# Kernel optimization log

Measured on AMD Instinct MI355X. Metric: run time of the kernel, lower is better.

Reference implementation:

```python
import jax, jax.numpy as jnp
import numpy as np

B, C, H, W = 8, 64, 64, 64


def setup_inputs() -> dict:
    key = jax.random.key(0)
    ks = jax.random.split(key, 8)
    s = 1.0 / np.sqrt(C)  # keep logits in a reasonable range
    return {
        "x": jax.random.normal(ks[0], (B, C, H, W), dtype=jnp.float32),
        "Wf": jax.random.normal(ks[1], (C, C), dtype=jnp.float32) * s,
        "bf": jax.random.normal(ks[2], (C,), dtype=jnp.float32) * s,
        "Wg": jax.random.normal(ks[3], (C, C), dtype=jnp.float32) * s,
        "bg": jax.random.normal(ks[4], (C,), dtype=jnp.float32) * s,
        "Wh": jax.random.normal(ks[5], (C, C), dtype=jnp.float32) * s,
        "bh": jax.random.normal(ks[6], (C,), dtype=jnp.float32) * s,
        "gamma": jax.random.normal(ks[7], (1,), dtype=jnp.float32),
    }


def reference(x, Wf, bf, Wg, bg, Wh, bh, gamma):
    b, c, h, w = x.shape
    n = h * w
    xf = x.reshape(b, c, n)  # [B, C, N]
    # 1x1 convs == per-pixel channel GEMMs
    f = jnp.einsum("oc,bcn->bon", Wf, xf) + bf[None, :, None]  # [B, C, N]
    g = jnp.einsum("oc,bcn->bon", Wg, xf) + bg[None, :, None]
    hh = jnp.einsum("oc,bcn->bon", Wh, xf) + bh[None, :, None]
    # att_in[b, i, j] = f[b, :, i] . g[b, :, j]  (f_x permuted then bmm with g_x)
    att = jax.nn.softmax(jnp.einsum("bci,bcj->bij", f, g), axis=-1)  # [B, N, N]
    # torch.bmm(h_x, attention): out[b, c, j] = sum_i h[b, c, i] * att[b, i, j]
    out = jnp.einsum("bci,bij->bcj", hh, att).reshape(b, c, h, w)
    return gamma[0] * out + x
```

## Files before the change

### kernel.cpp

```cpp
#include <hip/hip_runtime.h>

#define BB 8
#define CC 64
#define NN 4096
#define NIC 4
#define JCH 8
#define LOG2E 1.4426950408889634f

typedef float f32x4  __attribute__((ext_vector_type(4)));
typedef float f32x16 __attribute__((ext_vector_type(16)));
typedef _Float16 half8_t __attribute__((ext_vector_type(8)));
typedef int int4v __attribute__((ext_vector_type(4)));


__global__ __launch_bounds__(256, 4) void qkv_kernel(
    const float* __restrict__ x,
    const float* __restrict__ Wf, const float* __restrict__ bf,
    const float* __restrict__ Wg, const float* __restrict__ bg,
    const float* __restrict__ Wh, const float* __restrict__ bh,
    _Float16* __restrict__ fT, _Float16* __restrict__ gT,
    _Float16* __restrict__ hT)
{
    __shared__ float xbuf[64][136];

    const int tid  = threadIdx.x;
    const int lane = tid & 63;
    const int wv   = tid >> 6;
    const int l31  = lane & 31;
    const int q5   = lane >> 5;
    const int n0   = blockIdx.x * 128;
    const int b    = blockIdx.y;
    const int z    = blockIdx.z;
    const float* W    = (z == 0) ? Wf : ((z == 1) ? Wg : Wh);
    const float* bias = (z == 0) ? bf : ((z == 1) ? bg : bh);

    {
        const int row = tid >> 2;
        const float* src = x + (size_t)(b * CC + row) * NN + n0 + (tid & 3) * 4;
#pragma unroll
        for (int k = 0; k < 8; ++k) {
            const f32x4 v = *(const f32x4*)(src + k * 16);
            *(f32x4*)&xbuf[row][(tid & 3) * 4 + k * 16] = v;
        }
    }
    __syncthreads();

    const int px = wv * 32 + l31;
    half8_t xf[4];
#pragma unroll
    for (int kc = 0; kc < 4; ++kc) {
        const int kb = kc * 16 + q5 * 8;
        int4v p;
#pragma unroll
        for (int h2 = 0; h2 < 4; ++h2) {
            p[h2] = __builtin_bit_cast(int, __builtin_amdgcn_cvt_pkrtz(
                xbuf[kb + h2 * 2][px], xbuf[kb + h2 * 2 + 1][px]));
        }
        xf[kc] = __builtin_bit_cast(half8_t, p);
    }

    half8_t wf[2][4];
#pragma unroll
    for (int ot = 0; ot < 2; ++ot) {
        const float* wrow = W + (size_t)(ot * 32 + l31) * CC;
#pragma unroll
        for (int kc = 0; kc < 4; ++kc) {
            const f32x4 w0 = *(const f32x4*)(wrow + kc * 16 + q5 * 8);
            const f32x4 w1 = *(const f32x4*)(wrow + kc * 16 + q5 * 8 + 4);
            int4v p;
            p[0] = __builtin_bit_cast(int, __builtin_amdgcn_cvt_pkrtz(w0[0], w0[1]));
            p[1] = __builtin_bit_cast(int, __builtin_amdgcn_cvt_pkrtz(w0[2], w0[3]));
            p[2] = __builtin_bit_cast(int, __builtin_amdgcn_cvt_pkrtz(w1[0], w1[1]));
            p[3] = __builtin_bit_cast(int, __builtin_amdgcn_cvt_pkrtz(w1[2], w1[3]));
            wf[ot][kc] = __builtin_bit_cast(half8_t, p);
        }
    }

    if (z < 2) {
        const float scale = (z == 0) ? LOG2E : 1.0f;
        _Float16* dstT = (z == 0) ? fT : gT;
#pragma unroll
        for (int ot = 0; ot < 2; ++ot) {
            f32x16 acc = {};
#pragma unroll
            for (int kc = 0; kc < 4; ++kc)
                acc = __builtin_amdgcn_mfma_f32_32x32x16_f16(xf[kc], wf[ot][kc], acc, 0, 0, 0);
            const float bv = bias[ot * 32 + l31];
#pragma unroll
            for (int r = 0; r < 16; ++r) {
                const int prow = (r & 3) + 8 * (r >> 2) + 4 * q5;
                const int n = n0 + wv * 32 + prow;
                dstT[(size_t)(b * NN + n) * CC + ot * 32 + l31] =
                    (_Float16)((acc[r] + bv) * scale);
            }
        }
    } else {
        _Float16* hbase = hT + ((size_t)(b * (NN / 32) + (n0 + wv * 32) / 32) * CC) * 32;
#pragma unroll
        for (int ot = 0; ot < 2; ++ot) {
            f32x16 acc = {};
#pragma unroll
            for (int kc = 0; kc < 4; ++kc)
                acc = __builtin_amdgcn_mfma_f32_32x32x16_f16(wf[ot][kc], xf[kc], acc, 0, 0, 0);
#pragma unroll
            for (int rb = 0; rb < 4; ++rb) {
                const f32x4 b4 = *(const f32x4*)(bias + ot * 32 + rb * 8 + q5 * 4);
#pragma unroll
                for (int k = 0; k < 4; ++k) {
                    const int c = ot * 32 + rb * 8 + q5 * 4 + k;
                    hbase[(size_t)c * 32 + l31] = (_Float16)(acc[rb * 4 + k] + b4[k]);
                }
            }
        }
    }
}

__global__ __launch_bounds__(256, 4) void stats_kernel(
    const _Float16* __restrict__ fT, const _Float16* __restrict__ gT,
    float* __restrict__ lpart)
{
    __shared__ _Float16 gbuf[2][64][72];

    const int lane = threadIdx.x & 63;
    const int wv   = threadIdx.x >> 6;
    const int b    = blockIdx.y;
    const int jc   = blockIdx.z;
    const int i0   = blockIdx.x * 128 + wv * 32;
    const int l31  = lane & 31;
    const int q5   = lane >> 5;

    half8_t a[4];
    const _Float16* fa = fT + (size_t)(b * NN + i0 + l31) * CC + q5 * 8;
#pragma unroll
    for (int kc = 0; kc < 4; ++kc) a[kc] = *(const half8_t*)(fa + kc * 16);

    const _Float16* gchunk = gT + (size_t)(b * NN + jc * (NN / JCH)) * CC;
    const int T = NN / JCH / 64;

    const int srow = wv * 16 + (lane >> 3);
    const int scol = (lane & 7) * 8;

    {
        const half8_t v0 = *(const half8_t*)(gchunk + (size_t)srow * CC + scol);
        const half8_t v1 = *(const half8_t*)(gchunk + (size_t)(srow + 8) * CC + scol);
        *(half8_t*)&gbuf[0][srow][scol] = v0;
        *(half8_t*)&gbuf[0][srow + 8][scol] = v1;
    }
    __syncthreads();

    float l16[16];
#pragma unroll
    for (int r = 0; r < 16; ++r) l16[r] = 0.f;

    for (int t = 0; t < T; ++t) {
        const int buf = t & 1;
        const bool pf = (t + 1 < T);
        half8_t p0, p1;
        if (pf) {
            const _Float16* src = gchunk + (size_t)((t + 1) * 64 + srow) * CC + scol;
            p0 = *(const half8_t*)(src);
            p1 = *(const half8_t*)(src + 8 * CC);
        }
#pragma unroll
        for (int js = 0; js < 2; ++js) {
            const _Float16* grow = &gbuf[buf][js * 32 + l31][0] + q5 * 8;
            f32x16 s = {};
#pragma unroll
            for (int kc = 0; kc < 4; ++kc) {
                const half8_t bfr = *(const half8_t*)(grow + kc * 16);
                s = __builtin_amdgcn_mfma_f32_32x32x16_f16(a[kc], bfr, s, 0, 0, 0);
            }
#pragma unroll
            for (int r = 0; r < 16; ++r) l16[r] += __builtin_exp2f(s[r]);
        }
        if (pf) {
            *(half8_t*)&gbuf[buf ^ 1][srow][scol] = p0;
            *(half8_t*)&gbuf[buf ^ 1][srow + 8][scol] = p1;
        }
        __syncthreads();
    }

#pragma unroll
    for (int r = 0; r < 16; ++r) {
#pragma unroll
        for (int off = 1; off < 32; off <<= 1)
            l16[r] += __shfl_xor(l16[r], off);
    }

    if (l31 == 0) {
        float* lp = lpart + (size_t)jc * BB * NN + b * NN + i0;
#pragma unroll
        for (int rb = 0; rb < 4; ++rb) {
            f32x4 v;
#pragma unroll
            for (int k = 0; k < 4; ++k) v[k] = l16[rb * 4 + k];
            *(f32x4*)(lp + rb * 8 + q5 * 4) = v;
        }
    }
}

__global__ __launch_bounds__(256) void rmerge_kernel(
    const float* __restrict__ lpart, float* __restrict__ nbias)
{
    const int idx = blockIdx.x * 256 + threadIdx.x;
    float s = 0.f;
#pragma unroll
    for (int jc = 0; jc < JCH; ++jc) s += lpart[(size_t)jc * BB * NN + idx];
    nbias[idx] = -__builtin_log2f(s);
}

__global__ __launch_bounds__(256, 2) void attn_kernel(
    const _Float16* __restrict__ fT, const _Float16* __restrict__ gT,
    const _Float16* __restrict__ hT, const float* __restrict__ nbias,
    _Float16* __restrict__ pout)
{
    __shared__ _Float16 fbuf[2][64][72];
    __shared__ _Float16 hbuf[2][64][72];

    const int lane = threadIdx.x & 63;
    const int wv   = threadIdx.x >> 6;
    const int b    = blockIdx.y;
    const int ic   = blockIdx.z;
    const int l31  = lane & 31;
    const int q5   = lane >> 5;
    const int jbase = blockIdx.x * 256 + wv * 64;

    half8_t bg[2][4];
#pragma unroll
    for (int jt = 0; jt < 2; ++jt) {
        const _Float16* grow = gT + (size_t)(b * NN + jbase + jt * 32 + l31) * CC + q5 * 8;
#pragma unroll
        for (int kc = 0; kc < 4; ++kc) bg[jt][kc] = *(const half8_t*)(grow + kc * 16);
    }

    f32x16 acc[2][2] = {};

    const int ichunk = NN / NIC;
    const int ibase  = ic * ichunk;
    const _Float16* fchunk = fT + ((size_t)b * NN + ibase) * CC;
    const _Float16* hchunk = hT + ((size_t)(b * (NN / 32) + ibase / 32) * CC) * 32;
    const float*    nb     = nbias + b * NN + ibase;
    const int T = ichunk / 64;

    const int tid    = threadIdx.x;
    const int frow_s = tid >> 2;
    const int fcol_s = (tid & 3) * 16;
    const int hrow_s = tid >> 2;
    const int hcol_s = (tid & 3) * 8;

    {
        const half8_t f0 = *(const half8_t*)(fchunk + (size_t)frow_s * CC + fcol_s);
        const half8_t f1 = *(const half8_t*)(fchunk + (size_t)frow_s * CC + fcol_s + 8);
        const half8_t h0 = *(const half8_t*)(hchunk + tid * 8);
        const half8_t h1 = *(const half8_t*)(hchunk + 2048 + tid * 8);
        *(half8_t*)&fbuf[0][frow_s][fcol_s]     = f0;
        *(half8_t*)&fbuf[0][frow_s][fcol_s + 8] = f1;
        *(half8_t*)&hbuf[0][hrow_s][hcol_s]      = h0;
        *(half8_t*)&hbuf[0][hrow_s][32 + hcol_s] = h1;
    }
    __syncthreads();

    for (int t = 0; t < T; ++t) {
        const int buf = t & 1;
        const bool pf = (t + 1 < T);
        half8_t pf0, pf1, ph0, ph1;
        if (pf) {
            const _Float16* fsrc = fchunk + (size_t)((t + 1) * 64 + frow_s) * CC + fcol_s;
            const _Float16* hsrc = hchunk + (size_t)(t + 1) * 4096 + tid * 8;
            pf0 = *(const half8_t*)(fsrc);
            pf1 = *(const half8_t*)(fsrc + 8);
            ph0 = *(const half8_t*)(hsrc);
            ph1 = *(const half8_t*)(hsrc + 2048);
        }

#pragma unroll
        for (int ih = 0; ih < 2; ++ih) {
            f32x16 s0;
#pragma unroll
            for (int rb = 0; rb < 4; ++rb) {
                const f32x4 n4 = *(const f32x4*)(nb + t * 64 + ih * 32 + rb * 8 + q5 * 4);
#pragma unroll
                for (int k = 0; k < 4; ++k) s0[rb * 4 + k] = n4[k];
            }
            f32x16 s1 = s0;
            const _Float16* frow = &fbuf[buf][ih * 32 + l31][0] + q5 * 8;
#pragma unroll
            for (int kc = 0; kc < 4; ++kc) {
                const half8_t af = *(const half8_t*)(frow + kc * 16);
                s0 = __builtin_amdgcn_mfma_f32_32x32x16_f16(af, bg[0][kc], s0, 0, 0, 0);
                s1 = __builtin_amdgcn_mfma_f32_32x32x16_f16(af, bg[1][kc], s1, 0, 0, 0);
            }

            half8_t B[2][2];
#pragma unroll
            for (int jt = 0; jt < 2; ++jt) {
                const f32x16& s = jt ? s1 : s0;
                int e[8];
#pragma unroll
                for (int r8 = 0; r8 < 8; ++r8) {
                    e[r8] = __builtin_bit_cast(int, __builtin_amdgcn_cvt_pkrtz(
                        __builtin_exp2f(s[r8 * 2]), __builtin_exp2f(s[r8 * 2 + 1])));
                }
                const int sA = q5 ? e[0] : e[2];
                const int sB = q5 ? e[1] : e[3];
                const int sC = q5 ? e[4] : e[6];
                const int sD = q5 ? e[5] : e[7];
                const int rA = __shfl_xor(sA, 32, 64);
                const int rB = __shfl_xor(sB, 32, 64);
                const int rC = __shfl_xor(sC, 32, 64);
                const int rD = __shfl_xor(sD, 32, 64);
                int4v b0, b1;
                b0[0] = q5 ? rA   : e[0];
                b0[1] = q5 ? rB   : e[1];
                b0[2] = q5 ? e[2] : rA;
                b0[3] = q5 ? e[3] : rB;
                b1[0] = q5 ? rC   : e[4];
                b1[1] = q5 ? rD   : e[5];
                b1[2] = q5 ? e[6] : rC;
                b1[3] = q5 ? e[7] : rD;
                B[jt][0] = __builtin_bit_cast(half8_t, b0);
                B[jt][1] = __builtin_bit_cast(half8_t, b1);
            }

#pragma unroll
            for (int ct = 0; ct < 2; ++ct) {
                const half8_t ah0 = *(const half8_t*)(&hbuf[buf][ct * 32 + l31][0] + ih * 32 + q5 * 8);
                const half8_t ah1 = *(const half8_t*)(&hbuf[buf][ct * 32 + l31][0] + ih * 32 + 16 + q5 * 8);
                acc[0][ct] = __builtin_amdgcn_mfma_f32_32x32x16_f16(ah0, B[0][0], acc[0][ct], 0, 0, 0);
                acc[0][ct] = __builtin_amdgcn_mfma_f32_32x32x16_f16(ah1, B[0][1], acc[0][ct], 0, 0, 0);
                acc[1][ct] = __builtin_amdgcn_mfma_f32_32x32x16_f16(ah0, B[1][0], acc[1][ct], 0, 0, 0);
                acc[1][ct] = __builtin_amdgcn_mfma_f32_32x32x16_f16(ah1, B[1][1], acc[1][ct], 0, 0, 0);
            }
        }

        if (pf) {
            *(half8_t*)&fbuf[buf ^ 1][frow_s][fcol_s]     = pf0;
            *(half8_t*)&fbuf[buf ^ 1][frow_s][fcol_s + 8] = pf1;
            *(half8_t*)&hbuf[buf ^ 1][hrow_s][hcol_s]      = ph0;
            *(half8_t*)&hbuf[buf ^ 1][hrow_s][32 + hcol_s] = ph1;
        }
        __syncthreads();
    }

    _Float16* pb_out = pout + (((size_t)ic * BB + b) * CC) * NN;
#pragma unroll
    for (int jt = 0; jt < 2; ++jt) {
        const int j = jbase + jt * 32 + l31;
#pragma unroll
        for (int ct = 0; ct < 2; ++ct) {
#pragma unroll
            for (int r = 0; r < 16; ++r) {
                const int c = ct * 32 + (r & 3) + 8 * (r >> 2) + 4 * q5;
                pb_out[(size_t)c * NN + j] = (_Float16)acc[jt][ct][r];
            }
        }
    }
}

__global__ __launch_bounds__(256) void combine_kernel(
    const float* __restrict__ x, const float* __restrict__ gammap,
    const _Float16* __restrict__ pout, float* __restrict__ out)
{
    const float gam = gammap[0];
    const size_t i8 = ((size_t)blockIdx.x * 256 + threadIdx.x) * 8;
    const size_t TOT = (size_t)BB * CC * NN;

    float s[8] = {0.f, 0.f, 0.f, 0.f, 0.f, 0.f, 0.f, 0.f};
#pragma unroll
    for (int ic = 0; ic < NIC; ++ic) {
        const half8_t p = *(const half8_t*)(pout + ic * TOT + i8);
#pragma unroll
        for (int k = 0; k < 8; ++k) s[k] += (float)p[k];
    }
    const f32x4 x0 = *(const f32x4*)(x + i8);
    const f32x4 x1 = *(const f32x4*)(x + i8 + 4);
    f32x4 o0, o1;
#pragma unroll
    for (int k = 0; k < 4; ++k) { o0[k] = gam * s[k] + x0[k]; o1[k] = gam * s[k + 4] + x1[k]; }
    *(f32x4*)(out + i8) = o0;
    *(f32x4*)(out + i8 + 4) = o1;
}

extern "C" void kernel_launch(void* const* d_in, const int* in_sizes, int n_in,
                              void* d_out, int out_size, void* d_ws, size_t ws_size,
                              hipStream_t stream) {
    const float* x     = (const float*)d_in[0];
    const float* Wf    = (const float*)d_in[1];
    const float* bf    = (const float*)d_in[2];
    const float* Wg    = (const float*)d_in[3];
    const float* bg    = (const float*)d_in[4];
    const float* Wh    = (const float*)d_in[5];
    const float* bh    = (const float*)d_in[6];
    const float* gamma = (const float*)d_in[7];
    float* out = (float*)d_out;

    const size_t TOT = (size_t)BB * CC * NN;
    _Float16* fT   = (_Float16*)d_ws;
    _Float16* gT   = fT + TOT;
    _Float16* hT   = gT + TOT;
    _Float16* pout = hT + TOT;
    float* lpart   = (float*)(pout + (size_t)NIC * TOT);
    float* nbias   = lpart + (size_t)JCH * BB * NN;

    qkv_kernel<<<dim3(NN / 128, BB, 3), 256, 0, stream>>>(
        x, Wf, bf, Wg, bg, Wh, bh, fT, gT, hT);
    stats_kernel<<<dim3(NN / 128, BB, JCH), 256, 0, stream>>>(fT, gT, lpart);
    rmerge_kernel<<<dim3(BB * NN / 256), 256, 0, stream>>>(lpart, nbias);
    attn_kernel<<<dim3(NN / 256, BB, NIC), 256, 0, stream>>>(fT, gT, hT, nbias, pout);
    combine_kernel<<<dim3(TOT / (256 * 8)), 256, 0, stream>>>(x, gamma, pout, out);
}
```

Baseline: 177.7 us.

## Fuse Q/K/V projections into one block so x is loaded once

New measurement: 177.5 us. Within noise of the previous version (-0.1%).

```diff
diff --git a/kernel.cpp b/kernel.cpp
--- a/kernel.cpp
+++ b/kernel.cpp
@@ -13,7 +13,7 @@
 typedef int int4v __attribute__((ext_vector_type(4)));
 
 
-__global__ __launch_bounds__(256, 4) void qkv_kernel(
+__global__ __launch_bounds__(256, 2) void qkv_kernel(
     const float* __restrict__ x,
     const float* __restrict__ Wf, const float* __restrict__ bf,
     const float* __restrict__ Wg, const float* __restrict__ bg,
@@ -21,31 +21,28 @@
     _Float16* __restrict__ fT, _Float16* __restrict__ gT,
     _Float16* __restrict__ hT)
 {
-    __shared__ float xbuf[64][136];
+    __shared__ float xbuf[64][68];
 
     const int tid  = threadIdx.x;
     const int lane = tid & 63;
     const int wv   = tid >> 6;
     const int l31  = lane & 31;
     const int q5   = lane >> 5;
-    const int n0   = blockIdx.x * 128;
+    const int st   = wv & 1;
+    const int zg   = wv >> 1;
+    const int n0   = blockIdx.x * 64;
     const int b    = blockIdx.y;
-    const int z    = blockIdx.z;
-    const float* W    = (z == 0) ? Wf : ((z == 1) ? Wg : Wh);
-    const float* bias = (z == 0) ? bf : ((z == 1) ? bg : bh);
 
     {
-        const int row = tid >> 2;
-        const float* src = x + (size_t)(b * CC + row) * NN + n0 + (tid & 3) * 4;
-#pragma unroll
-        for (int k = 0; k < 8; ++k) {
-            const f32x4 v = *(const f32x4*)(src + k * 16);
-            *(f32x4*)&xbuf[row][(tid & 3) * 4 + k * 16] = v;
-        }
+        const int c = tid >> 2;
+        const float* src = x + (size_t)(b * CC + c) * NN + n0 + (tid & 3) * 16;
+#pragma unroll
+        for (int k = 0; k < 4; ++k)
+            *(f32x4*)&xbuf[c][(tid & 3) * 16 + k * 4] = *(const f32x4*)(src + k * 4);
     }
     __syncthreads();
 
-    const int px = wv * 32 + l31;
+    const int pxl = st * 32 + l31;
     half8_t xf[4];
 #pragma unroll
     for (int kc = 0; kc < 4; ++kc) {
@@ -54,14 +51,12 @@
 #pragma unroll
         for (int h2 = 0; h2 < 4; ++h2) {
             p[h2] = __builtin_bit_cast(int, __builtin_amdgcn_cvt_pkrtz(
-                xbuf[kb + h2 * 2][px], xbuf[kb + h2 * 2 + 1][px]));
+                xbuf[kb + h2 * 2][pxl], xbuf[kb + h2 * 2 + 1][pxl]));
         }
         xf[kc] = __builtin_bit_cast(half8_t, p);
     }
 
-    half8_t wf[2][4];
-#pragma unroll
-    for (int ot = 0; ot < 2; ++ot) {
+    auto load_wf = [&](const float* W, int ot, half8_t* out) {
         const float* wrow = W + (size_t)(ot * 32 + l31) * CC;
 #pragma unroll
         for (int kc = 0; kc < 4; ++kc) {
@@ -72,39 +67,56 @@
             p[1] = __builtin_bit_cast(int, __builtin_amdgcn_cvt_pkrtz(w0[2], w0[3]));
             p[2] = __builtin_bit_cast(int, __builtin_amdgcn_cvt_pkrtz(w1[0], w1[1]));
             p[3] = __builtin_bit_cast(int, __builtin_amdgcn_cvt_pkrtz(w1[2], w1[3]));
-            wf[ot][kc] = __builtin_bit_cast(half8_t, p);
-        }
-    }
-
-    if (z < 2) {
-        const float scale = (z == 0) ? LOG2E : 1.0f;
-        _Float16* dstT = (z == 0) ? fT : gT;
+            out[kc] = __builtin_bit_cast(half8_t, p);
+        }
+    };
+
+    auto store_fg = [&](_Float16* dstT, const float* bias, int ot,
+                        const f32x16& acc, float scale) {
+        const float bv = bias[ot * 32 + l31];
+#pragma unroll
+        for (int r = 0; r < 16; ++r) {
+            const int prow = (r & 3) + 8 * (r >> 2) + 4 * q5;
+            const int n = n0 + st * 32 + prow;
+            dstT[(size_t)(b * NN + n) * CC + ot * 32 + l31] =
+                (_Float16)((acc[r] + bv) * scale);
+        }
+    };
+
+    if (zg == 0) {
+        half8_t wfa[4], wfb[4], wga[4];
+        load_wf(Wf, 0, wfa);
+        load_wf(Wf, 1, wfb);
+        load_wf(Wg, 0, wga);
+        f32x16 a0 = {}, a1 = {}, a2 = {};
+#pragma unroll
+        for (int kc = 0; kc < 4; ++kc) {
+            a0 = __builtin_amdgcn_mfma_f32_32x32x16_f16(xf[kc], wfa[kc], a0, 0, 0, 0);
+            a1 = __builtin_amdgcn_mfma_f32_32x32x16_f16(xf[kc], wfb[kc], a1, 0, 0, 0);
+            a2 = __builtin_amdgcn_mfma_f32_32x32x16_f16(xf[kc], wga[kc], a2, 0, 0, 0);
+        }
+        store_fg(fT, bf, 0, a0, LOG2E);
+        store_fg(fT, bf, 1, a1, LOG2E);
+        store_fg(gT, bg, 0, a2, 1.0f);
+    } else {
+        half8_t wha[4], whb[4], wgb[4];
+        load_wf(Wh, 0, wha);
+        load_wf(Wh, 1, whb);
+        load_wf(Wg, 1, wgb);
+        f32x16 a0 = {}, a1 = {}, a2 = {};
+#pragma unroll
+        for (int kc = 0; kc < 4; ++kc) {
+            a0 = __builtin_amdgcn_mfma_f32_32x32x16_f16(wha[kc], xf[kc], a0, 0, 0, 0);
+            a1 = __builtin_amdgcn_mfma_f32_32x32x16_f16(whb[kc], xf[kc], a1, 0, 0, 0);
+            a2 = __builtin_amdgcn_mfma_f32_32x32x16_f16(xf[kc], wgb[kc], a2, 0, 0, 0);
+        }
+        _Float16* hbase = hT + ((size_t)(b * (NN / 32) + (n0 + st * 32) / 32) * CC) * 32;
 #pragma unroll
         for (int ot = 0; ot < 2; ++ot) {
-            f32x16 acc = {};
-#pragma unroll
-            for (int kc = 0; kc < 4; ++kc)
-                acc = __builtin_amdgcn_mfma_f32_32x32x16_f16(xf[kc], wf[ot][kc], acc, 0, 0, 0);
-            const float bv = bias[ot * 32 + l31];
-#pragma unroll
-            for (int r = 0; r < 16; ++r) {
-                const int prow = (r & 3) + 8 * (r >> 2) + 4 * q5;
-                const int n = n0 + wv * 32 + prow;
-                dstT[(size_t)(b * NN + n) * CC + ot * 32 + l31] =
-                    (_Float16)((acc[r] + bv) * scale);
-            }
-        }
-    } else {
-        _Float16* hbase = hT + ((size_t)(b * (NN / 32) + (n0 + wv * 32) / 32) * CC) * 32;
-#pragma unroll
-        for (int ot = 0; ot < 2; ++ot) {
-            f32x16 acc = {};
-#pragma unroll
-            for (int kc = 0; kc < 4; ++kc)
-                acc = __builtin_amdgcn_mfma_f32_32x32x16_f16(wf[ot][kc], xf[kc], acc, 0, 0, 0);
+            const f32x16& acc = ot ? a1 : a0;
 #pragma unroll
             for (int rb = 0; rb < 4; ++rb) {
-                const f32x4 b4 = *(const f32x4*)(bias + ot * 32 + rb * 8 + q5 * 4);
+                const f32x4 b4 = *(const f32x4*)(bh + ot * 32 + rb * 8 + q5 * 4);
 #pragma unroll
                 for (int k = 0; k < 4; ++k) {
                     const int c = ot * 32 + rb * 8 + q5 * 4 + k;
@@ -112,6 +124,7 @@
                 }
             }
         }
+        store_fg(gT, bg, 1, a2, 1.0f);
     }
 }
 
@@ -402,7 +415,7 @@
     float* lpart   = (float*)(pout + (size_t)NIC * TOT);
     float* nbias   = lpart + (size_t)JCH * BB * NN;
 
-    qkv_kernel<<<dim3(NN / 128, BB, 3), 256, 0, stream>>>(
+    qkv_kernel<<<dim3(NN / 64, BB), 256, 0, stream>>>(
         x, Wf, bf, Wg, bg, Wh, bh, fT, gT, hT);
     stats_kernel<<<dim3(NN / 128, BB, JCH), 256, 0, stream>>>(fT, gT, lpart);
     rmerge_kernel<<<dim3(BB * NN / 256), 256, 0, stream>>>(lpart, nbias);
```

## Fuse row-sum merge into attention kernel and restructure QKV projection blocks

Applied to the files above, without the earlier changes.

After: 171.1 us. 1.04x faster.

```diff
diff --git a/kernel.cpp b/kernel.cpp
--- a/kernel.cpp
+++ b/kernel.cpp
@@ -13,7 +13,7 @@
 typedef int int4v __attribute__((ext_vector_type(4)));
 
 
-__global__ __launch_bounds__(256, 4) void qkv_kernel(
+__global__ __launch_bounds__(384, 6) void qkv_kernel(
     const float* __restrict__ x,
     const float* __restrict__ Wf, const float* __restrict__ bf,
     const float* __restrict__ Wg, const float* __restrict__ bg,
@@ -21,31 +21,27 @@
     _Float16* __restrict__ fT, _Float16* __restrict__ gT,
     _Float16* __restrict__ hT)
 {
-    __shared__ float xbuf[64][136];
+    __shared__ float xbuf[64][36];
 
     const int tid  = threadIdx.x;
     const int lane = tid & 63;
     const int wv   = tid >> 6;
     const int l31  = lane & 31;
     const int q5   = lane >> 5;
-    const int n0   = blockIdx.x * 128;
+    const int z    = wv >> 1;
+    const int ot   = wv & 1;
+    const int n0   = blockIdx.x * 32;
     const int b    = blockIdx.y;
-    const int z    = blockIdx.z;
-    const float* W    = (z == 0) ? Wf : ((z == 1) ? Wg : Wh);
-    const float* bias = (z == 0) ? bf : ((z == 1) ? bg : bh);
-
-    {
+
+    if (tid < 256) {
         const int row = tid >> 2;
-        const float* src = x + (size_t)(b * CC + row) * NN + n0 + (tid & 3) * 4;
-#pragma unroll
-        for (int k = 0; k < 8; ++k) {
-            const f32x4 v = *(const f32x4*)(src + k * 16);
-            *(f32x4*)&xbuf[row][(tid & 3) * 4 + k * 16] = v;
-        }
+        const int px4 = (tid & 3) * 8;
+        const float* src = x + (size_t)(b * CC + row) * NN + n0 + px4;
+        *(f32x4*)&xbuf[row][px4]     = *(const f32x4*)(src);
+        *(f32x4*)&xbuf[row][px4 + 4] = *(const f32x4*)(src + 4);
     }
     __syncthreads();
 
-    const int px = wv * 32 + l31;
     half8_t xf[4];
 #pragma unroll
     for (int kc = 0; kc < 4; ++kc) {
@@ -54,14 +50,16 @@
 #pragma unroll
         for (int h2 = 0; h2 < 4; ++h2) {
             p[h2] = __builtin_bit_cast(int, __builtin_amdgcn_cvt_pkrtz(
-                xbuf[kb + h2 * 2][px], xbuf[kb + h2 * 2 + 1][px]));
+                xbuf[kb + h2 * 2][l31], xbuf[kb + h2 * 2 + 1][l31]));
         }
         xf[kc] = __builtin_bit_cast(half8_t, p);
     }
 
-    half8_t wf[2][4];
-#pragma unroll
-    for (int ot = 0; ot < 2; ++ot) {
+    const float* W    = (z == 0) ? Wf : ((z == 1) ? Wg : Wh);
+    const float* bias = (z == 0) ? bf : ((z == 1) ? bg : bh);
+
+    half8_t wf[4];
+    {
         const float* wrow = W + (size_t)(ot * 32 + l31) * CC;
 #pragma unroll
         for (int kc = 0; kc < 4; ++kc) {
@@ -72,44 +70,37 @@
             p[1] = __builtin_bit_cast(int, __builtin_amdgcn_cvt_pkrtz(w0[2], w0[3]));
             p[2] = __builtin_bit_cast(int, __builtin_amdgcn_cvt_pkrtz(w1[0], w1[1]));
             p[3] = __builtin_bit_cast(int, __builtin_amdgcn_cvt_pkrtz(w1[2], w1[3]));
-            wf[ot][kc] = __builtin_bit_cast(half8_t, p);
+            wf[kc] = __builtin_bit_cast(half8_t, p);
         }
     }
 
     if (z < 2) {
+        f32x16 acc = {};
+#pragma unroll
+        for (int kc = 0; kc < 4; ++kc)
+            acc = __builtin_amdgcn_mfma_f32_32x32x16_f16(xf[kc], wf[kc], acc, 0, 0, 0);
+        _Float16* dstT = (z == 0) ? fT : gT;
         const float scale = (z == 0) ? LOG2E : 1.0f;
-        _Float16* dstT = (z == 0) ? fT : gT;
-#pragma unroll
-        for (int ot = 0; ot < 2; ++ot) {
-            f32x16 acc = {};
-#pragma unroll
-            for (int kc = 0; kc < 4; ++kc)
-                acc = __builtin_amdgcn_mfma_f32_32x32x16_f16(xf[kc], wf[ot][kc], acc, 0, 0, 0);
-            const float bv = bias[ot * 32 + l31];
-#pragma unroll
-            for (int r = 0; r < 16; ++r) {
-                const int prow = (r & 3) + 8 * (r >> 2) + 4 * q5;
-                const int n = n0 + wv * 32 + prow;
-                dstT[(size_t)(b * NN + n) * CC + ot * 32 + l31] =
-                    (_Float16)((acc[r] + bv) * scale);
-            }
+        const float bv = bias[ot * 32 + l31];
+#pragma unroll
+        for (int r = 0; r < 16; ++r) {
+            const int prow = (r & 3) + 8 * (r >> 2) + 4 * q5;
+            dstT[(size_t)(b * NN + n0 + prow) * CC + ot * 32 + l31] =
+                (_Float16)((acc[r] + bv) * scale);
         }
     } else {
-        _Float16* hbase = hT + ((size_t)(b * (NN / 32) + (n0 + wv * 32) / 32) * CC) * 32;
-#pragma unroll
-        for (int ot = 0; ot < 2; ++ot) {
-            f32x16 acc = {};
-#pragma unroll
-            for (int kc = 0; kc < 4; ++kc)
-                acc = __builtin_amdgcn_mfma_f32_32x32x16_f16(wf[ot][kc], xf[kc], acc, 0, 0, 0);
-#pragma unroll
-            for (int rb = 0; rb < 4; ++rb) {
-                const f32x4 b4 = *(const f32x4*)(bias + ot * 32 + rb * 8 + q5 * 4);
-#pragma unroll
-                for (int k = 0; k < 4; ++k) {
-                    const int c = ot * 32 + rb * 8 + q5 * 4 + k;
-                    hbase[(size_t)c * 32 + l31] = (_Float16)(acc[rb * 4 + k] + b4[k]);
-                }
+        f32x16 acc = {};
+#pragma unroll
+        for (int kc = 0; kc < 4; ++kc)
+            acc = __builtin_amdgcn_mfma_f32_32x32x16_f16(wf[kc], xf[kc], acc, 0, 0, 0);
+        _Float16* hbase = hT + ((size_t)(b * (NN / 32) + blockIdx.x) * CC) * 32;
+#pragma unroll
+        for (int rb = 0; rb < 4; ++rb) {
+            const f32x4 b4 = *(const f32x4*)(bias + ot * 32 + rb * 8 + q5 * 4);
+#pragma unroll
+            for (int k = 0; k < 4; ++k) {
+                const int c = ot * 32 + rb * 8 + q5 * 4 + k;
+                hbase[(size_t)c * 32 + l31] = (_Float16)(acc[rb * 4 + k] + b4[k]);
             }
         }
     }
@@ -199,23 +190,14 @@
     }
 }
 
-__global__ __launch_bounds__(256) void rmerge_kernel(
-    const float* __restrict__ lpart, float* __restrict__ nbias)
-{
-    const int idx = blockIdx.x * 256 + threadIdx.x;
-    float s = 0.f;
-#pragma unroll
-    for (int jc = 0; jc < JCH; ++jc) s += lpart[(size_t)jc * BB * NN + idx];
-    nbias[idx] = -__builtin_log2f(s);
-}
-
 __global__ __launch_bounds__(256, 2) void attn_kernel(
     const _Float16* __restrict__ fT, const _Float16* __restrict__ gT,
-    const _Float16* __restrict__ hT, const float* __restrict__ nbias,
+    const _Float16* __restrict__ hT, const float* __restrict__ lpart,
     _Float16* __restrict__ pout)
 {
     __shared__ _Float16 fbuf[2][64][72];
     __shared__ _Float16 hbuf[2][64][72];
+    __shared__ float nbbuf[NN / NIC];
 
     const int lane = threadIdx.x & 63;
     const int wv   = threadIdx.x >> 6;
@@ -225,6 +207,25 @@
     const int q5   = lane >> 5;
     const int jbase = blockIdx.x * 256 + wv * 64;
 
+    const int ichunk = NN / NIC;
+    const int ibase  = ic * ichunk;
+    const int tid    = threadIdx.x;
+
+    {
+        const float* lp0 = lpart + b * NN + ibase + tid * 4;
+        f32x4 sum = *(const f32x4*)(lp0);
+#pragma unroll
+        for (int jc = 1; jc < JCH; ++jc) {
+            const f32x4 v = *(const f32x4*)(lp0 + (size_t)jc * BB * NN);
+#pragma unroll
+            for (int k = 0; k < 4; ++k) sum[k] += v[k];
+        }
+        f32x4 nb4;
+#pragma unroll
+        for (int k = 0; k < 4; ++k) nb4[k] = -__builtin_log2f(sum[k]);
+        *(f32x4*)&nbbuf[tid * 4] = nb4;
+    }
+
     half8_t bg[2][4];
 #pragma unroll
     for (int jt = 0; jt < 2; ++jt) {
@@ -235,14 +236,10 @@
 
     f32x16 acc[2][2] = {};
 
-    const int ichunk = NN / NIC;
-    const int ibase  = ic * ichunk;
     const _Float16* fchunk = fT + ((size_t)b * NN + ibase) * CC;
     const _Float16* hchunk = hT + ((size_t)(b * (NN / 32) + ibase / 32) * CC) * 32;
-    const float*    nb     = nbias + b * NN + ibase;
     const int T = ichunk / 64;
 
-    const int tid    = threadIdx.x;
     const int frow_s = tid >> 2;
     const int fcol_s = (tid & 3) * 16;
     const int hrow_s = tid >> 2;
@@ -278,7 +275,7 @@
             f32x16 s0;
 #pragma unroll
             for (int rb = 0; rb < 4; ++rb) {
-                const f32x4 n4 = *(const f32x4*)(nb + t * 64 + ih * 32 + rb * 8 + q5 * 4);
+                const f32x4 n4 = *(const f32x4*)&nbbuf[t * 64 + ih * 32 + rb * 8 + q5 * 4];
 #pragma unroll
                 for (int k = 0; k < 4; ++k) s0[rb * 4 + k] = n4[k];
             }
@@ -400,12 +397,10 @@
     _Float16* hT   = gT + TOT;
     _Float16* pout = hT + TOT;
     float* lpart   = (float*)(pout + (size_t)NIC * TOT);
-    float* nbias   = lpart + (size_t)JCH * BB * NN;
-
-    qkv_kernel<<<dim3(NN / 128, BB, 3), 256, 0, stream>>>(
+
+    qkv_kernel<<<dim3(NN / 32, BB), 384, 0, stream>>>(
         x, Wf, bf, Wg, bg, Wh, bh, fT, gT, hT);
     stats_kernel<<<dim3(NN / 128, BB, JCH), 256, 0, stream>>>(fT, gT, lpart);
-    rmerge_kernel<<<dim3(BB * NN / 256), 256, 0, stream>>>(lpart, nbias);
-    attn_kernel<<<dim3(NN / 256, BB, NIC), 256, 0, stream>>>(fT, gT, hT, nbias, pout);
+    attn_kernel<<<dim3(NN / 256, BB, NIC), 256, 0, stream>>>(fT, gT, hT, lpart, pout);
     combine_kernel<<<dim3(TOT / (256 * 8)), 256, 0, stream>>>(x, gamma, pout, out);
 }
```
